# Kernel tuning notes

Measured on AMD Instinct MI355X. Metric: run time of the kernel, lower is better.

Reference implementation:

```python
import jax, jax.numpy as jnp
import numpy as np

EPS = 1e-12  # torch F.normalize eps


def setup_inputs() -> dict:
    key = jax.random.key(0)
    k1, k2, k3 = jax.random.split(key, 3)
    N, C, H, W = 64, 512, 30, 30
    K = 64
    x = jax.random.normal(k1, (N, C, H, W), dtype=jnp.float32)
    # 1x1 conv weight [K, C] (kernel spatial dims squeezed out)
    conv_w = jax.random.normal(k2, (K, C), dtype=jnp.float32) * 0.04
    centroids = jax.random.uniform(k3, (K, C), dtype=jnp.float32)
    return {"x": x, "conv_w": conv_w, "centroids": centroids}


def reference(x, conv_w, centroids):
    N, C, H, W = x.shape
    K = conv_w.shape[0]
    # descriptor-wise L2 normalize over channel dim (normalize_input=True)
    nrm = jnp.sqrt(jnp.sum(x * x, axis=1, keepdims=True))
    x = x / jnp.maximum(nrm, EPS)
    xf = x.reshape(N, C, H * W)                       # [N, C, P]
    # 1x1 conv == per-pixel matmul: [N, K, P]
    logits = jnp.einsum("kc,ncp->nkp", conv_w, xf)
    a = jax.nn.softmax(logits, axis=1)                # softmax over clusters
    # vlad[n,k,c] = sum_p a[n,k,p] * (xf[n,c,p] - centroids[k,c])
    #            = (a @ xf^T) - sum_p(a) * centroids   (GEMM decomposition)
    agg = jnp.einsum("nkp,ncp->nkc", a, xf)           # [N, K, C]
    vlad = agg - a.sum(axis=-1)[:, :, None] * centroids[None]
    return vlad
```

## Files before the change

### kernel.cpp

```cpp
#include <hip/hip_runtime.h>
#include <math.h>

#define N_DIM 64
#define C_DIM 512
#define K_DIM 64
#define P_DIM 900
#define P_PAD 928
#define PTILES 15

typedef __attribute__((ext_vector_type(8))) short short8;
typedef __attribute__((ext_vector_type(4))) float f32x4;
typedef __attribute__((ext_vector_type(4))) uint  u32x4;

#define A2_ELEMS   ((size_t)N_DIM * K_DIM * P_PAD)

__device__ inline ushort f2bf(float f) {
  uint u = __builtin_bit_cast(uint, f);
  u += 0x7FFFu + ((u >> 16) & 1u);
  return (ushort)(u >> 16);
}
__device__ inline uint pk2(float a, float b) {
  return (uint)f2bf(a) | ((uint)f2bf(b) << 16);
}

__device__ __forceinline__ void gload16(const float* g, float* lds_base) {
  __builtin_amdgcn_global_load_lds(
      (const __attribute__((address_space(1))) void*)g,
      (__attribute__((address_space(3))) void*)lds_base, 16, 0, 0);
}

__global__ __launch_bounds__(256, 2) void netvlad_assign(
    const float* __restrict__ x, const float* __restrict__ w,
    ushort* __restrict__ a2, float* __restrict__ asum_part)
{
  const int n = blockIdx.y, bpt = blockIdx.x, p0 = bpt * 64;
  const int tid = threadIdx.x, wv = tid >> 6, lane = tid & 63;
  const int l15 = lane & 15, lhi = lane >> 4;

  __shared__ float xs[2][8192];
  __shared__ float wredm[4][4][16];
  __shared__ float wreds[4][4][16];

  short8 wfrag[16];
  const float* wrow = w + (size_t)(wv * 16 + l15) * C_DIM + lhi * 8;
#pragma unroll
  for (int ks = 0; ks < 16; ++ks) {
    f32x4 f0 = *(const f32x4*)(wrow + ks * 32);
    f32x4 f1 = *(const f32x4*)(wrow + ks * 32 + 4);
    u32x4 up;
    up[0] = pk2(f0[0], f0[1]); up[1] = pk2(f0[2], f0[3]);
    up[2] = pk2(f1[0], f1[1]); up[3] = pk2(f1[2], f1[3]);
    wfrag[ks] = __builtin_bit_cast(short8, up);
  }

  const float* xb = x + (size_t)n * C_DIM * P_DIM;
  int pld = p0 + (lane & 15) * 4;
  if (pld > P_DIM - 4) pld = P_DIM - 4;
  const int rquad = lane >> 4;

#define STAGE(b, ch)                                                           \
  {                                                                            \
    _Pragma("unroll")                                                          \
    for (int i = 0; i < 8; ++i) {                                              \
      int seg = wv + 4 * i;                                                    \
      int rr  = (ch) * 128 + seg * 4 + rquad;                                  \
      gload16(xb + (size_t)rr * P_DIM + pld, &xs[b][seg * 256]);               \
    }                                                                          \
  }

  f32x4 acc[4];
#pragma unroll
  for (int pt = 0; pt < 4; ++pt) acc[pt] = (f32x4){0.f, 0.f, 0.f, 0.f};
  float ssqp[4] = {0.f, 0.f, 0.f, 0.f};

  STAGE(0, 0);
#pragma unroll
  for (int ch = 0; ch < 4; ++ch) {
    if (ch + 1 < 4) STAGE((ch + 1) & 1, ch + 1);
    if (ch < 3) asm volatile("s_waitcnt vmcnt(8)" ::: "memory");
    else        asm volatile("s_waitcnt vmcnt(0)" ::: "memory");
    __builtin_amdgcn_sched_barrier(0);
    __builtin_amdgcn_s_barrier();
    const float* buf = xs[ch & 1];
#pragma unroll
    for (int ks = 0; ks < 4; ++ks) {
      f32x4 rd[8];
#pragma unroll
      for (int j = 0; j < 8; ++j)
        rd[j] = *(const f32x4*)&buf[(ks * 32 + 8 * lhi + j) * 64 + l15 * 4];
#pragma unroll
      for (int pt = 0; pt < 4; ++pt) {
        ssqp[pt] += rd[0][pt] * rd[0][pt] + rd[1][pt] * rd[1][pt]
                  + rd[2][pt] * rd[2][pt] + rd[3][pt] * rd[3][pt]
                  + rd[4][pt] * rd[4][pt] + rd[5][pt] * rd[5][pt]
                  + rd[6][pt] * rd[6][pt] + rd[7][pt] * rd[7][pt];
        u32x4 up;
        up[0] = pk2(rd[0][pt], rd[1][pt]); up[1] = pk2(rd[2][pt], rd[3][pt]);
        up[2] = pk2(rd[4][pt], rd[5][pt]); up[3] = pk2(rd[6][pt], rd[7][pt]);
        short8 xf = __builtin_bit_cast(short8, up);
        acc[pt] = __builtin_amdgcn_mfma_f32_16x16x32_bf16(
                      wfrag[ch * 4 + ks], xf, acc[pt], 0, 0, 0);
      }
    }
    __builtin_amdgcn_s_barrier();
  }
#undef STAGE

  float linv[4];
#pragma unroll
  for (int pt = 0; pt < 4; ++pt) {
    float s = ssqp[pt];
    s += __shfl_xor(s, 16);
    s += __shfl_xor(s, 32);
    linv[pt] = 1.0f / fmaxf(sqrtf(s), 1e-12f);
  }

  float lg[4][4];
#pragma unroll
  for (int pt = 0; pt < 4; ++pt) {
    float m = -1e30f;
#pragma unroll
    for (int r = 0; r < 4; ++r) { lg[pt][r] = acc[pt][r] * linv[pt]; m = fmaxf(m, lg[pt][r]); }
    m = fmaxf(m, __shfl_xor(m, 16));
    m = fmaxf(m, __shfl_xor(m, 32));
    if (lhi == 0) wredm[wv][pt][l15] = m;
  }
  __syncthreads();
#pragma unroll
  for (int pt = 0; pt < 4; ++pt) {
    float m = fmaxf(fmaxf(wredm[0][pt][l15], wredm[1][pt][l15]),
                    fmaxf(wredm[2][pt][l15], wredm[3][pt][l15]));
    float s = 0.f;
#pragma unroll
    for (int r = 0; r < 4; ++r) { lg[pt][r] = __expf(lg[pt][r] - m); s += lg[pt][r]; }
    s += __shfl_xor(s, 16);
    s += __shfl_xor(s, 32);
    if (lhi == 0) wreds[wv][pt][l15] = s;
  }
  __syncthreads();

  ushort* a2b = a2 + (size_t)n * K_DIM * P_PAD;
  float asr[4] = {0.f, 0.f, 0.f, 0.f};
#pragma unroll
  for (int pt = 0; pt < 4; ++pt) {
    float stot = wreds[0][pt][l15] + wreds[1][pt][l15] +
                 wreds[2][pt][l15] + wreds[3][pt][l15];
    float rs = 1.0f / stot;
    int p = p0 + 4 * l15 + pt;
    bool vv = p < P_DIM;
#pragma unroll
    for (int r = 0; r < 4; ++r) {
      float a = lg[pt][r] * rs;
      if (vv) asr[r] += a;
      if (p < P_PAD) {
        int k = wv * 16 + lhi * 4 + r;
        a2b[(size_t)k * P_PAD + p] = vv ? f2bf(a * linv[pt]) : (ushort)0;
      }
    }
  }
#pragma unroll
  for (int r = 0; r < 4; ++r) {
    float v = asr[r];
    v += __shfl_xor(v, 1); v += __shfl_xor(v, 2);
    v += __shfl_xor(v, 4); v += __shfl_xor(v, 8);
    if (l15 == 0) {
      int k = wv * 16 + lhi * 4 + r;
      asum_part[((size_t)n * K_DIM + k) * PTILES + bpt] = v;
    }
  }
}

__global__ __launch_bounds__(256, 4) void netvlad_agg(
    const float* __restrict__ x, const ushort* __restrict__ a2,
    const float* __restrict__ asum_part, const float* __restrict__ cent,
    float* __restrict__ out)
{
  const int n = blockIdx.y, ct = blockIdx.x, c0 = ct * 64;
  const int tid = threadIdx.x, wave = tid >> 6, lane = tid & 63;
  const int l15 = lane & 15, lhi = lane >> 4;

  __shared__ float asum_s[64];
  if (tid < 64) {
    const float* ap = asum_part + ((size_t)n * K_DIM + tid) * PTILES;
    float s = 0.f;
#pragma unroll
    for (int j = 0; j < PTILES; ++j) s += ap[j];
    asum_s[tid] = s;
  }
  __syncthreads();

  f32x4 acc[4];
#pragma unroll
  for (int mt = 0; mt < 4; ++mt) acc[mt] = (f32x4){0.f, 0.f, 0.f, 0.f};

  const float*  xrow = x + (size_t)n * C_DIM * P_DIM
                         + (size_t)(c0 + wave * 16 + l15) * P_DIM;
  const ushort* ab   = a2 + (size_t)n * K_DIM * P_PAD;

  for (int ks = 0; ks < 29; ++ks) {
    int pb = ks * 32 + lhi * 8;
    short8 bfrag;
    if (pb + 8 <= P_DIM) {
      f32x4 f0 = *(const f32x4*)(xrow + pb);
      f32x4 f1 = *(const f32x4*)(xrow + pb + 4);
      u32x4 up;
      up[0] = pk2(f0[0], f0[1]); up[1] = pk2(f0[2], f0[3]);
      up[2] = pk2(f1[0], f1[1]); up[3] = pk2(f1[2], f1[3]);
      bfrag = __builtin_bit_cast(short8, up);
    } else {
#pragma unroll
      for (int j = 0; j < 8; ++j)
        bfrag[j] = (pb + j < P_DIM) ? (short)f2bf(xrow[pb + j]) : (short)0;
    }
#pragma unroll
    for (int mt = 0; mt < 4; ++mt) {
      short8 afrag = *(const short8*)(ab + (size_t)(mt * 16 + l15) * P_PAD
                                         + ks * 32 + lhi * 8);
      acc[mt] = __builtin_amdgcn_mfma_f32_16x16x32_bf16(afrag, bfrag, acc[mt], 0, 0, 0);
    }
  }

  const int c = c0 + wave * 16 + l15;
#pragma unroll
  for (int mt = 0; mt < 4; ++mt) {
#pragma unroll
    for (int r = 0; r < 4; ++r) {
      int k = mt * 16 + lhi * 4 + r;
      out[((size_t)n * K_DIM + k) * C_DIM + c] =
          acc[mt][r] - asum_s[k] * cent[(size_t)k * C_DIM + c];
    }
  }
}

extern "C" void kernel_launch(void* const* d_in, const int* in_sizes, int n_in,
                              void* d_out, int out_size, void* d_ws, size_t ws_size,
                              hipStream_t stream) {
  const float* x    = (const float*)d_in[0];
  const float* w    = (const float*)d_in[1];
  const float* cent = (const float*)d_in[2];
  float* out = (float*)d_out;

  ushort* a2        = (ushort*)d_ws;
  float*  asum_part = (float*)((char*)d_ws + A2_ELEMS * sizeof(ushort));

  netvlad_assign<<<dim3(PTILES, N_DIM), 256, 0, stream>>>(x, w, a2, asum_part);
  netvlad_agg   <<<dim3(8, N_DIM),      256, 0, stream>>>(x, a2, asum_part, cent, out);
}
```

Measured before the change: 81.32 us.

## Halve assign pixel tile, stream conv weights per chunk, swizzle LDS staging

The assign kernel now handles 32 pixels per block instead of 64, so there are 29 pixel tiles and twice as many blocks. Shared memory drops to 16 KB per buffer and launch bounds rise to 4 blocks per CU. Conv weights are no longer all held in registers. Each chunk's weights are loaded alongside the next x stage and converted to bf16 after the current MFMAs, which cuts register pressure. LDS writes use an XOR swizzle to reduce bank conflicts on the 2-float reads, at the cost of more per-block overhead, more redundant weight loads and more asum partials for the agg kernel to sum.

```diff
diff --git a/kernel.cpp b/kernel.cpp
--- a/kernel.cpp
+++ b/kernel.cpp
@@ -6,11 +6,12 @@
 #define K_DIM 64
 #define P_DIM 900
 #define P_PAD 928
-#define PTILES 15
+#define PTILES 29
 
 typedef __attribute__((ext_vector_type(8))) short short8;
 typedef __attribute__((ext_vector_type(4))) float f32x4;
 typedef __attribute__((ext_vector_type(4))) uint  u32x4;
+typedef __attribute__((ext_vector_type(2))) float f32x2;
 
 #define A2_ELEMS   ((size_t)N_DIM * K_DIM * P_PAD)
 
@@ -29,67 +30,88 @@
       (__attribute__((address_space(3))) void*)lds_base, 16, 0, 0);
 }
 
-__global__ __launch_bounds__(256, 2) void netvlad_assign(
+__global__ __launch_bounds__(256, 4) void netvlad_assign(
     const float* __restrict__ x, const float* __restrict__ w,
     ushort* __restrict__ a2, float* __restrict__ asum_part)
 {
-  const int n = blockIdx.y, bpt = blockIdx.x, p0 = bpt * 64;
+  const int n = blockIdx.y, bpt = blockIdx.x, p0 = bpt * 32;
   const int tid = threadIdx.x, wv = tid >> 6, lane = tid & 63;
   const int l15 = lane & 15, lhi = lane >> 4;
-
-  __shared__ float xs[2][8192];
-  __shared__ float wredm[4][4][16];
-  __shared__ float wreds[4][4][16];
-
-  short8 wfrag[16];
+  const int r8 = lane >> 3, g = lane & 7;
+
+  __shared__ float xs[2][4096];
+  __shared__ float wredm[4][2][16];
+  __shared__ float wreds[4][2][16];
+
+  const float* xb = x + (size_t)n * C_DIM * P_DIM;
   const float* wrow = w + (size_t)(wv * 16 + l15) * C_DIM + lhi * 8;
-#pragma unroll
-  for (int ks = 0; ks < 16; ++ks) {
-    f32x4 f0 = *(const f32x4*)(wrow + ks * 32);
-    f32x4 f1 = *(const f32x4*)(wrow + ks * 32 + 4);
-    u32x4 up;
-    up[0] = pk2(f0[0], f0[1]); up[1] = pk2(f0[2], f0[3]);
-    up[2] = pk2(f1[0], f1[1]); up[3] = pk2(f1[2], f1[3]);
-    wfrag[ks] = __builtin_bit_cast(short8, up);
-  }
-
-  const float* xb = x + (size_t)n * C_DIM * P_DIM;
-  int pld = p0 + (lane & 15) * 4;
-  if (pld > P_DIM - 4) pld = P_DIM - 4;
-  const int rquad = lane >> 4;
 
 #define STAGE(b, ch)                                                           \
   {                                                                            \
     _Pragma("unroll")                                                          \
-    for (int i = 0; i < 8; ++i) {                                              \
-      int seg = wv + 4 * i;                                                    \
-      int rr  = (ch) * 128 + seg * 4 + rquad;                                  \
-      gload16(xb + (size_t)rr * P_DIM + pld, &xs[b][seg * 256]);               \
+    for (int i = 0; i < 4; ++i) {                                              \
+      int rl  = wv * 32 + i * 8;                                               \
+      int swz = (wv * 4 + i) & 7;                                              \
+      int pld = p0 + ((g ^ swz) << 2);                                         \
+      if (pld > P_DIM - 4) pld = P_DIM - 4;                                    \
+      gload16(xb + (size_t)((ch) * 128 + rl + r8) * P_DIM + pld,               \
+              &xs[b][rl * 32]);                                                \
     }                                                                          \
   }
 
-  f32x4 acc[4];
-#pragma unroll
-  for (int pt = 0; pt < 4; ++pt) acc[pt] = (f32x4){0.f, 0.f, 0.f, 0.f};
-  float ssqp[4] = {0.f, 0.f, 0.f, 0.f};
+  f32x4 acc[2];
+  acc[0] = (f32x4){0.f, 0.f, 0.f, 0.f};
+  acc[1] = (f32x4){0.f, 0.f, 0.f, 0.f};
+  float ssqp[2] = {0.f, 0.f};
+  short8 wf[4];
 
   STAGE(0, 0);
+  {
+    f32x4 wr[8];
+#pragma unroll
+    for (int kl = 0; kl < 4; ++kl) {
+      wr[2 * kl]     = *(const f32x4*)(wrow + kl * 32);
+      wr[2 * kl + 1] = *(const f32x4*)(wrow + kl * 32 + 4);
+    }
+#pragma unroll
+    for (int kl = 0; kl < 4; ++kl) {
+      u32x4 up;
+      up[0] = pk2(wr[2 * kl][0], wr[2 * kl][1]);
+      up[1] = pk2(wr[2 * kl][2], wr[2 * kl][3]);
+      up[2] = pk2(wr[2 * kl + 1][0], wr[2 * kl + 1][1]);
+      up[3] = pk2(wr[2 * kl + 1][2], wr[2 * kl + 1][3]);
+      wf[kl] = __builtin_bit_cast(short8, up);
+    }
+  }
+
 #pragma unroll
   for (int ch = 0; ch < 4; ++ch) {
-    if (ch + 1 < 4) STAGE((ch + 1) & 1, ch + 1);
-    if (ch < 3) asm volatile("s_waitcnt vmcnt(8)" ::: "memory");
-    else        asm volatile("s_waitcnt vmcnt(0)" ::: "memory");
+    f32x4 wrn[8];
+    if (ch + 1 < 4) {
+      STAGE((ch + 1) & 1, ch + 1);
+#pragma unroll
+      for (int kl = 0; kl < 4; ++kl) {
+        wrn[2 * kl]     = *(const f32x4*)(wrow + ((ch + 1) * 4 + kl) * 32);
+        wrn[2 * kl + 1] = *(const f32x4*)(wrow + ((ch + 1) * 4 + kl) * 32 + 4);
+      }
+      asm volatile("s_waitcnt vmcnt(12)" ::: "memory");
+    } else {
+      asm volatile("s_waitcnt vmcnt(0)" ::: "memory");
+    }
     __builtin_amdgcn_sched_barrier(0);
     __builtin_amdgcn_s_barrier();
-    const float* buf = xs[ch & 1];
-#pragma unroll
-    for (int ks = 0; ks < 4; ++ks) {
-      f32x4 rd[8];
+
+    const char* buf = (const char*)xs[ch & 1];
+#pragma unroll
+    for (int kl = 0; kl < 4; ++kl) {
+      const int swz = ((kl * 4 + lhi) & 7) << 4;
+      f32x2 rd[8];
 #pragma unroll
       for (int j = 0; j < 8; ++j)
-        rd[j] = *(const f32x4*)&buf[(ks * 32 + 8 * lhi + j) * 64 + l15 * 4];
-#pragma unroll
-      for (int pt = 0; pt < 4; ++pt) {
+        rd[j] = *(const f32x2*)(buf + (kl * 32 + lhi * 8 + j) * 128
+                                    + ((l15 * 8) ^ swz));
+#pragma unroll
+      for (int pt = 0; pt < 2; ++pt) {
         ssqp[pt] += rd[0][pt] * rd[0][pt] + rd[1][pt] * rd[1][pt]
                   + rd[2][pt] * rd[2][pt] + rd[3][pt] * rd[3][pt]
                   + rd[4][pt] * rd[4][pt] + rd[5][pt] * rd[5][pt]
@@ -98,26 +120,36 @@
         up[0] = pk2(rd[0][pt], rd[1][pt]); up[1] = pk2(rd[2][pt], rd[3][pt]);
         up[2] = pk2(rd[4][pt], rd[5][pt]); up[3] = pk2(rd[6][pt], rd[7][pt]);
         short8 xf = __builtin_bit_cast(short8, up);
-        acc[pt] = __builtin_amdgcn_mfma_f32_16x16x32_bf16(
-                      wfrag[ch * 4 + ks], xf, acc[pt], 0, 0, 0);
+        acc[pt] = __builtin_amdgcn_mfma_f32_16x16x32_bf16(wf[kl], xf, acc[pt], 0, 0, 0);
       }
     }
+    if (ch + 1 < 4) {
+#pragma unroll
+      for (int kl = 0; kl < 4; ++kl) {
+        u32x4 up;
+        up[0] = pk2(wrn[2 * kl][0], wrn[2 * kl][1]);
+        up[1] = pk2(wrn[2 * kl][2], wrn[2 * kl][3]);
+        up[2] = pk2(wrn[2 * kl + 1][0], wrn[2 * kl + 1][1]);
+        up[3] = pk2(wrn[2 * kl + 1][2], wrn[2 * kl + 1][3]);
+        wf[kl] = __builtin_bit_cast(short8, up);
+      }
+    }
     __builtin_amdgcn_s_barrier();
   }
 #undef STAGE
 
-  float linv[4];
-#pragma unroll
-  for (int pt = 0; pt < 4; ++pt) {
+  float linv[2];
+#pragma unroll
+  for (int pt = 0; pt < 2; ++pt) {
     float s = ssqp[pt];
     s += __shfl_xor(s, 16);
     s += __shfl_xor(s, 32);
     linv[pt] = 1.0f / fmaxf(sqrtf(s), 1e-12f);
   }
 
-  float lg[4][4];
-#pragma unroll
-  for (int pt = 0; pt < 4; ++pt) {
+  float lg[2][4];
+#pragma unroll
+  for (int pt = 0; pt < 2; ++pt) {
     float m = -1e30f;
 #pragma unroll
     for (int r = 0; r < 4; ++r) { lg[pt][r] = acc[pt][r] * linv[pt]; m = fmaxf(m, lg[pt][r]); }
@@ -127,7 +159,7 @@
   }
   __syncthreads();
 #pragma unroll
-  for (int pt = 0; pt < 4; ++pt) {
+  for (int pt = 0; pt < 2; ++pt) {
     float m = fmaxf(fmaxf(wredm[0][pt][l15], wredm[1][pt][l15]),
                     fmaxf(wredm[2][pt][l15], wredm[3][pt][l15]));
     float s = 0.f;
@@ -142,20 +174,18 @@
   ushort* a2b = a2 + (size_t)n * K_DIM * P_PAD;
   float asr[4] = {0.f, 0.f, 0.f, 0.f};
 #pragma unroll
-  for (int pt = 0; pt < 4; ++pt) {
+  for (int pt = 0; pt < 2; ++pt) {
     float stot = wreds[0][pt][l15] + wreds[1][pt][l15] +
                  wreds[2][pt][l15] + wreds[3][pt][l15];
     float rs = 1.0f / stot;
-    int p = p0 + 4 * l15 + pt;
+    int p = p0 + 2 * l15 + pt;
     bool vv = p < P_DIM;
 #pragma unroll
     for (int r = 0; r < 4; ++r) {
       float a = lg[pt][r] * rs;
       if (vv) asr[r] += a;
-      if (p < P_PAD) {
-        int k = wv * 16 + lhi * 4 + r;
-        a2b[(size_t)k * P_PAD + p] = vv ? f2bf(a * linv[pt]) : (ushort)0;
-      }
+      int k = wv * 16 + lhi * 4 + r;
+      a2b[(size_t)k * P_PAD + p] = vv ? f2bf(a * linv[pt]) : (ushort)0;
     }
   }
 #pragma unroll
@@ -183,7 +213,6 @@
   if (tid < 64) {
     const float* ap = asum_part + ((size_t)n * K_DIM + tid) * PTILES;
     float s = 0.f;
-#pragma unroll
     for (int j = 0; j < PTILES; ++j) s += ap[j];
     asum_s[tid] = s;
   }
```

Result: slower. 83.10 us (+2.2%).
